# Kernel tuning notes

Hardware: AMD Instinct MI355X
Metric: run time of the kernel (lower is better)

Reference implementation:

```python
import jax, jax.numpy as jnp
import numpy as np

D_MODEL = 1024
N_HEADS = 16
HEAD_DIM = D_MODEL // N_HEADS
B, S = 2, 2048


def setup_inputs() -> dict:
    key = jax.random.key(0)
    ks = jax.random.split(key, 6)
    w_scale = 1.0 / np.sqrt(D_MODEL)
    return {
        "query": jax.random.normal(ks[0], (B, S, D_MODEL), dtype=jnp.float32),
        "Wq": jax.random.normal(ks[1], (D_MODEL, D_MODEL), dtype=jnp.float32) * w_scale,
        "Wk": jax.random.normal(ks[2], (D_MODEL, D_MODEL), dtype=jnp.float32) * w_scale,
        "Wv": jax.random.normal(ks[3], (D_MODEL, D_MODEL), dtype=jnp.float32) * w_scale,
        "Wo": jax.random.normal(ks[4], (D_MODEL, D_MODEL), dtype=jnp.float32) * w_scale,
        "bo": jnp.zeros((D_MODEL,), dtype=jnp.float32),
    }


def reference(query, Wq, Wk, Wv, Wo, bo):
    # Self-attention: key = value = query (forward() defaults).
    b, t, _ = query.shape
    # Q/K/V projections (nn.Linear applies x @ W.T; weights here are stored as
    # [out, in] like torch, so project with W.T). Split into heads: [B,H,T,Dh].
    def proj(x, W):
        return (x @ W.T).reshape(b, t, N_HEADS, HEAD_DIM).transpose(0, 2, 1, 3)

    q = proj(query, Wq)
    k = proj(query, Wk)
    v = proj(query, Wv)

    scale = 1.0 / np.sqrt(HEAD_DIM)
    scores = jnp.einsum("bhqd,bhkd->bhqk", q, k) * scale  # [B,H,T,T]
    # Causal mask (is_causal=True, not cross-attention).
    causal = jnp.tril(jnp.ones((t, t), dtype=bool))
    scores = jnp.where(causal, scores, jnp.finfo(scores.dtype).min)
    weights = jax.nn.softmax(scores, axis=-1)
    out = jnp.einsum("bhqk,bhkd->bhqd", weights, v)  # [B,H,T,Dh]
    out = out.transpose(0, 2, 1, 3).reshape(b, t, D_MODEL)
    # Output projection with bias (dropout is identity in eval mode).
    return out @ Wo.T + bo
```

## Files before the change

### kernel.cpp

```cpp
#include <hip/hip_runtime.h>
#include <hip/hip_bf16.h>
#include <math.h>

typedef __attribute__((ext_vector_type(8))) short short8;
typedef __attribute__((ext_vector_type(4))) float floatx4;
typedef __attribute__((ext_vector_type(2))) _Float16 half2v;
typedef __attribute__((ext_vector_type(4))) _Float16 half4v;

#define MFMA_BF16_32(a, b, c) __builtin_amdgcn_mfma_f32_16x16x32_bf16(a, b, c, 0, 0, 0)
#define MFMA_F16_16(a, b, c) __builtin_amdgcn_mfma_f32_16x16x16f16(a, b, c, 0, 0, 0)

static constexpr int NH = 16;
static constexpr int Bb = 2;
static constexpr int Ss = 2048;
static constexpr int DM = 1024;

__device__ inline unsigned short f2bf(float f) {
    unsigned int u = __float_as_uint(f);
    u += 0x7fffu + ((u >> 16) & 1u);
    return (unsigned short)(u >> 16);
}

__device__ __forceinline__ half2v pkrtz(float a, float b) {
    return __builtin_bit_cast(half2v, __builtin_amdgcn_cvt_pkrtz(a, b));
}

__device__ __forceinline__ void gload_lds16(const unsigned short* g, unsigned short* l) {
    __builtin_amdgcn_global_load_lds(
        (const __attribute__((address_space(1))) unsigned int*)g,
        (__attribute__((address_space(3))) unsigned int*)l, 16, 0, 0);
}

__global__ void convert_all(const float* __restrict__ X, const float* __restrict__ w0,
                            const float* __restrict__ w1, const float* __restrict__ w2,
                            const float* __restrict__ w3, unsigned short* __restrict__ dstX,
                            unsigned short* __restrict__ dstW) {
    const int bid = blockIdx.x;
    const float* src;
    unsigned short* dst;
    int i;
    if (bid < 4096) {
        src = X; dst = dstX; i = bid * 256 + threadIdx.x;
    } else {
        const int w = (bid - 4096) >> 10;
        src = (w == 0) ? w0 : (w == 1) ? w1 : (w == 2) ? w2 : w3;
        dst = dstW + (size_t)w * 1048576;
        i = ((bid - 4096) & 1023) * 256 + threadIdx.x;
    }
    float4 v = ((const float4*)src)[i];
    ushort4 o;
    o.x = f2bf(v.x); o.y = f2bf(v.y); o.z = f2bf(v.z); o.w = f2bf(v.w);
    ((ushort4*)dst)[i] = o;
}

__global__ __launch_bounds__(256) void gemm_qkv(const unsigned short* __restrict__ A,
                                                const unsigned short* __restrict__ Bm,
                                                unsigned short* __restrict__ Qp,
                                                unsigned short* __restrict__ Kp,
                                                unsigned short* __restrict__ Vt) {
    __shared__ __align__(16) unsigned short As[2][4096];
    __shared__ __align__(16) unsigned short Bs[2][4096];
    const int K = 1024;
    const int tid = threadIdx.x;
    const int wave = tid >> 6, lane = tid & 63;
    const int quad = lane >> 4, l16 = lane & 15;
    const int wr = wave >> 1, wc = wave & 1;

    const int l = blockIdx.x;
    const int xcd = l & 7, slot = l >> 3;
    const int bx = (xcd & 3) * 8 + (slot & 7);
    const int by = (xcd >> 2) * 12 + (slot >> 3);
    const int bm = bx * 128;
    const int bn = by * 128;

    const int s0 = wave * 64 + lane;
    const int srow = s0 >> 2;
    const int scg = (s0 & 3) ^ ((srow >> 1) & 3);
    const unsigned short* gA0 = A + (size_t)(bm + srow) * K + scg * 8;
    const unsigned short* gB0 = Bm + (size_t)(bn + srow) * K + scg * 8;

    auto stage = [&](int k0, int buf) {
        gload_lds16(gA0 + k0, &As[buf][wave * 512]);
        gload_lds16(gA0 + (size_t)64 * K + k0, &As[buf][2048 + wave * 512]);
        gload_lds16(gB0 + k0, &Bs[buf][wave * 512]);
        gload_lds16(gB0 + (size_t)64 * K + k0, &Bs[buf][2048 + wave * 512]);
    };

    floatx4 acc[4][4];
#pragma unroll
    for (int i = 0; i < 4; i++)
#pragma unroll
        for (int j = 0; j < 4; j++) acc[i][j] = (floatx4)0.0f;

    stage(0, 0);
    int buf = 0;
    for (int k0 = 0; k0 < K; k0 += 32) {
        __syncthreads();
        if (k0 + 32 < K) stage(k0 + 32, buf ^ 1);
        short8 af[4];
#pragma unroll
        for (int im = 0; im < 4; im++) {
            const int frow = wr * 64 + im * 16 + l16;
            af[im] = *(const short8*)&As[buf][frow * 32 + ((quad ^ ((frow >> 1) & 3)) * 8)];
        }
#pragma unroll
        for (int jn = 0; jn < 4; jn++) {
            const int frow = wc * 64 + jn * 16 + l16;
            short8 bf = *(const short8*)&Bs[buf][frow * 32 + ((quad ^ ((frow >> 1) & 3)) * 8)];
#pragma unroll
            for (int im = 0; im < 4; im++) acc[im][jn] = MFMA_BF16_32(af[im], bf, acc[im][jn]);
        }
        buf ^= 1;
    }
    __syncthreads();

    unsigned short* LB = &As[0][0];

    if (by < 16) {
        unsigned short* dst = (by < 8) ? Qp : Kp;
        const int nb = (by & 7) * 128;
        const float scale = (by < 8) ? 0.125f : 1.0f;
#pragma unroll
        for (int hf = 0; hf < 2; ++hf) {
            if (wc == hf) {
#pragma unroll
                for (int im = 0; im < 4; im++)
#pragma unroll
                    for (int jn = 0; jn < 4; jn++) {
                        const int row = wr * 64 + im * 16 + quad * 4;
                        const int col = jn * 16 + l16;
#pragma unroll
                        for (int r = 0; r < 4; r++)
                            LB[(row + r) * 64 + col] = f2bf(acc[im][jn][r] * scale);
                    }
            }
            __syncthreads();
#pragma unroll
            for (int i = 0; i < 4; ++i) {
                const int flat = i * 256 + tid;
                const int row = flat >> 3, ch = flat & 7;
                short8 v = *(const short8*)&LB[row * 64 + ch * 8];
                *(short8*)&dst[(size_t)(bm + row) * 1024 + nb + hf * 64 + ch * 8] = v;
            }
            __syncthreads();
        }
    } else {
        _Float16* LF = (_Float16*)LB;
        const int dbase = (by - 16) * 128;
        const int bI = bm >> 11, sbase = bm & 2047;
#pragma unroll
        for (int hf = 0; hf < 2; ++hf) {
            if (wc == hf) {
#pragma unroll
                for (int im = 0; im < 4; im++)
#pragma unroll
                    for (int jn = 0; jn < 4; jn++) {
                        const int d64 = jn * 16 + l16;
                        const int sl = wr * 64 + im * 16 + quad * 4;
                        *(half2v*)&LF[d64 * 128 + sl] = pkrtz(acc[im][jn][0], acc[im][jn][1]);
                        *(half2v*)&LF[d64 * 128 + sl + 2] = pkrtz(acc[im][jn][2], acc[im][jn][3]);
                    }
            }
            __syncthreads();
#pragma unroll
            for (int i = 0; i < 4; ++i) {
                const int flat = i * 256 + tid;
                const int dr = flat >> 4, ch = flat & 15;
                short8 v = *(const short8*)&LF[dr * 128 + ch * 8];
                const int d = dbase + hf * 64 + dr;
                const int head = d >> 6, d64g = d & 63;
                *(short8*)&Vt[(((size_t)(bI * 16 + head)) * 64 + d64g) * 2048 + sbase + ch * 8] = v;
            }
            __syncthreads();
        }
    }
}

__global__ __launch_bounds__(256) void gemm_out(const unsigned short* __restrict__ A,
                                                const unsigned short* __restrict__ Bm,
                                                float* __restrict__ C,
                                                const float* __restrict__ bias) {
    __shared__ __align__(16) unsigned short As[2][8192];
    __shared__ __align__(16) unsigned short Bs[2][4096];
    const int K = 1024;
    const int tid = threadIdx.x;
    const int wave = tid >> 6, lane = tid & 63;
    const int quad = lane >> 4, l16 = lane & 15;

    const int l = blockIdx.x;
    const int xcd = l & 7, slot = l >> 3;
    const int bx = (xcd & 3) * 8 + (slot & 7);
    const int by = (xcd >> 2) * 8 + (slot >> 3);
    const int bm = bx * 128, bn = by * 64;

    const int s0 = wave * 64 + lane;
    const int srow = s0 >> 2;
    const int scg = (s0 & 3) ^ ((srow >> 1) & 3);
    const unsigned short* gA0 = A + (size_t)(bm + srow) * K + scg * 8;
    const unsigned short* gB0 = Bm + (size_t)(bn + srow) * K + scg * 8;

    auto stage = [&](int k0, int buf) {
#pragma unroll
        for (int kh = 0; kh < 2; ++kh) {
            gload_lds16(gA0 + k0 + kh * 32, &As[buf][kh * 4096 + wave * 512]);
            gload_lds16(gA0 + (size_t)64 * K + k0 + kh * 32,
                        &As[buf][kh * 4096 + 2048 + wave * 512]);
            gload_lds16(gB0 + k0 + kh * 32, &Bs[buf][kh * 2048 + wave * 512]);
        }
    };

    floatx4 acc[2][4];
#pragma unroll
    for (int i = 0; i < 2; i++)
#pragma unroll
        for (int j = 0; j < 4; j++) acc[i][j] = (floatx4)0.0f;

    stage(0, 0);
    int buf = 0;
    for (int k0 = 0; k0 < K; k0 += 64) {
        __syncthreads();
        if (k0 + 64 < K) stage(k0 + 64, buf ^ 1);
#pragma unroll
        for (int kh = 0; kh < 2; ++kh) {
            const int abase = kh * 4096, bbase = kh * 2048;
            short8 af[2];
#pragma unroll
            for (int im = 0; im < 2; im++) {
                const int frow = wave * 32 + im * 16 + l16;
                af[im] = *(const short8*)&As[buf][abase + frow * 32 +
                                                  ((quad ^ ((frow >> 1) & 3)) * 8)];
            }
#pragma unroll
            for (int jn = 0; jn < 4; jn++) {
                const int frow = jn * 16 + l16;
                short8 bf = *(const short8*)&Bs[buf][bbase + frow * 32 +
                                                     ((quad ^ ((frow >> 1) & 3)) * 8)];
#pragma unroll
                for (int im = 0; im < 2; im++) acc[im][jn] = MFMA_BF16_32(af[im], bf, acc[im][jn]);
            }
        }
        buf ^= 1;
    }

#pragma unroll
    for (int im = 0; im < 2; im++) {
#pragma unroll
        for (int jn = 0; jn < 4; jn++) {
            const int row0 = bm + wave * 32 + im * 16 + quad * 4;
            const int colg = bn + jn * 16 + l16;
            const float bv = bias[colg];
#pragma unroll
            for (int r = 0; r < 4; r++)
                C[(size_t)(row0 + r) * 1024 + colg] = acc[im][jn][r] + bv;
        }
    }
}

__global__ __launch_bounds__(256) void flash_attn(const unsigned short* __restrict__ Qp,
                                                  const unsigned short* __restrict__ Kp,
                                                  const _Float16* __restrict__ Vt,
                                                  unsigned short* __restrict__ Out) {
    __shared__ __align__(16) unsigned short Ks[2][4096];
    __shared__ __align__(16) _Float16 Vs[2][4096];
    const int bx = blockIdx.x, h = blockIdx.y, b = blockIdx.z;
    int qt = (bx + h) & 15;
    if (b) qt = 15 - qt;
    const int tid = threadIdx.x, w = tid >> 6, lane = tid & 63;
    const int quad = lane >> 4, l16 = lane & 15;

    const int t8 = tid >> 3;
    const int cg = (tid & 7) ^ (t8 & 7);
    const unsigned short* gK0 = Kp + ((size_t)(b * 2048 + t8) << 10) + h * 64 + cg * 8;
    const unsigned short* gK1 = gK0 + ((size_t)32 << 10);
    const _Float16* gV0 = Vt + ((size_t)((b * 16 + h) * 64 + t8) << 11) + cg * 8;
    const _Float16* gV1 = gV0 + ((size_t)32 << 11);
    unsigned short* ldsK = &Ks[0][0] + w * 512;
    _Float16* ldsV = &Vs[0][0] + w * 512;

    auto stage = [&](int kt, int buf) {
        const size_t ko = (size_t)kt << 16;
        const size_t vo = (size_t)kt << 6;
        gload_lds16(gK0 + ko, ldsK + buf * 4096);
        gload_lds16(gK1 + ko, ldsK + buf * 4096 + 2048);
        gload_lds16((const unsigned short*)(gV0 + vo), (unsigned short*)(ldsV + buf * 4096));
        gload_lds16((const unsigned short*)(gV1 + vo), (unsigned short*)(ldsV + buf * 4096 + 2048));
    };

    stage(0, 0);

    short8 qfA[2], qfB[2];
    {
        const unsigned short* qa =
            Qp + ((size_t)(b * 2048 + qt * 128 + w * 16 + l16) << 10) + h * 64 + quad * 8;
        qfA[0] = *(const short8*)qa;
        qfA[1] = *(const short8*)(qa + 32);
        const unsigned short* qb = qa + ((size_t)64 << 10);
        qfB[0] = *(const short8*)qb;
        qfB[1] = *(const short8*)(qb + 32);
    }

    floatx4 accA[4], accB[4];
#pragma unroll
    for (int dt = 0; dt < 4; dt++) { accA[dt] = (floatx4)0.0f; accB[dt] = (floatx4)0.0f; }
    float lA = 0.0f, lB = 0.0f;
    const int qloc = w * 16 + l16;
    const int sw = l16 & 7;
    const int ktEnd = 2 * qt + 1;

    for (int kt = 0; kt <= ktEnd; ++kt) {
        __syncthreads();
        const int buf = kt & 1;
        if (kt < ktEnd) stage(kt + 1, buf ^ 1);
        const bool aAct = (kt <= 2 * qt);
        const bool aDiag = (kt == 2 * qt);
        const bool bDiag = (kt == ktEnd);
        const unsigned short* KB = &Ks[buf][0];
        const _Float16* VB = &Vs[buf][0];

#pragma unroll
        for (int sc = 0; sc < 4; ++sc) {
            const int rowk = sc * 16 + l16;
            short8 kf0 = *(const short8*)&KB[rowk * 64 + ((quad ^ sw) * 8)];
            short8 kf1 = *(const short8*)&KB[rowk * 64 + (((4 + quad) ^ sw) * 8)];

            half4v pA, pB;
            if (aAct) {
                floatx4 sA = MFMA_BF16_32(kf0, qfA[0], (floatx4)(-2.0f));
                sA = MFMA_BF16_32(kf1, qfA[1], sA);
                float ps[4];
#pragma unroll
                for (int r = 0; r < 4; ++r) {
                    float e = __expf(sA[r]);
                    if (aDiag && (sc * 16 + quad * 4 + r > qloc)) e = 0.0f;
                    ps[r] = e;
                }
                lA += (ps[0] + ps[1]) + (ps[2] + ps[3]);
                pA = __builtin_shufflevector(pkrtz(ps[0], ps[1]), pkrtz(ps[2], ps[3]), 0, 1, 2, 3);
            }
            {
                floatx4 sB = MFMA_BF16_32(kf0, qfB[0], (floatx4)(-2.0f));
                sB = MFMA_BF16_32(kf1, qfB[1], sB);
                float ps[4];
#pragma unroll
                for (int r = 0; r < 4; ++r) {
                    float e = __expf(sB[r]);
                    if (bDiag && (sc * 16 + quad * 4 + r > qloc)) e = 0.0f;
                    ps[r] = e;
                }
                lB += (ps[0] + ps[1]) + (ps[2] + ps[3]);
                pB = __builtin_shufflevector(pkrtz(ps[0], ps[1]), pkrtz(ps[2], ps[3]), 0, 1, 2, 3);
            }

#pragma unroll
            for (int dt = 0; dt < 4; ++dt) {
                const int rowv = dt * 16 + l16;
                const int cgv = ((sc * 2 + (quad >> 1)) ^ sw);
                half4v vf = *(const half4v*)&VB[rowv * 64 + cgv * 8 + (quad & 1) * 4];
                if (aAct) accA[dt] = MFMA_F16_16(vf, pA, accA[dt]);
                accB[dt] = MFMA_F16_16(vf, pB, accB[dt]);
            }
        }
    }

    lA += __shfl_xor(lA, 16); lA += __shfl_xor(lA, 32);
    lB += __shfl_xor(lB, 16); lB += __shfl_xor(lB, 32);
    const float iA = 1.0f / lA;
    const float iB = 1.0f / lB;

    const size_t rowA = (size_t)(b * 2048 + qt * 128 + w * 16 + l16);
    const size_t rowB = rowA + 64;
#pragma unroll
    for (int dt = 0; dt < 4; ++dt) {
        const int col = h * 64 + dt * 16 + quad * 4;
        ushort4 oa, ob;
        oa.x = f2bf(accA[dt][0] * iA); oa.y = f2bf(accA[dt][1] * iA);
        oa.z = f2bf(accA[dt][2] * iA); oa.w = f2bf(accA[dt][3] * iA);
        ob.x = f2bf(accB[dt][0] * iB); ob.y = f2bf(accB[dt][1] * iB);
        ob.z = f2bf(accB[dt][2] * iB); ob.w = f2bf(accB[dt][3] * iB);
        *(ushort4*)&Out[rowA * 1024 + col] = oa;
        *(ushort4*)&Out[rowB * 1024 + col] = ob;
    }
}

extern "C" void kernel_launch(void* const* d_in, const int* in_sizes, int n_in,
                              void* d_out, int out_size, void* d_ws, size_t ws_size,
                              hipStream_t stream) {
    const float* X  = (const float*)d_in[0];
    const float* Wq = (const float*)d_in[1];
    const float* Wk = (const float*)d_in[2];
    const float* Wv = (const float*)d_in[3];
    const float* Wo = (const float*)d_in[4];
    const float* bo = (const float*)d_in[5];

    unsigned short* ws = (unsigned short*)d_ws;
    unsigned short* Xb   = ws;
    unsigned short* W4   = ws + (size_t)4194304;
    unsigned short* Wob  = W4 + (size_t)3145728;
    unsigned short* Qp   = ws + (size_t)8388608;
    unsigned short* Kp   = ws + (size_t)12582912;
    unsigned short* Vt   = ws + (size_t)16777216;
    unsigned short* At   = ws + (size_t)20971520;

    convert_all<<<8192, 256, 0, stream>>>(X, Wq, Wk, Wv, Wo, Xb, W4);

    gemm_qkv<<<768, 256, 0, stream>>>(Xb, W4, Qp, Kp, Vt);

    flash_attn<<<dim3(16, NH, Bb), 256, 0, stream>>>(Qp, Kp, (const _Float16*)Vt, At);

    gemm_out<<<512, 256, 0, stream>>>(At, Wob, (float*)d_out, bo);
}
```

Before: 200.8 us.

## Triple-buffer LDS staging with vmcnt barriers and XCD-aware attention block mapping

Converts the double-buffered global-to-LDS pipelines in both GEMMs and flash attention to triple buffering. The full __syncthreads is replaced by an s_waitcnt vmcnt(N)+s_barrier so loads two stages ahead can stay in flight. This aims to hide memory latency behind the MFMA work. The attention launch also becomes a 1D grid remapped so each XCD handles whole (batch, head) pairs with balanced causal work. The cost is more LDS per block, which may reduce occupancy, and the code now relies on exact vmcnt counts.

```diff
diff --git a/kernel.cpp b/kernel.cpp
--- a/kernel.cpp
+++ b/kernel.cpp
@@ -9,6 +9,10 @@
 
 #define MFMA_BF16_32(a, b, c) __builtin_amdgcn_mfma_f32_16x16x32_bf16(a, b, c, 0, 0, 0)
 #define MFMA_F16_16(a, b, c) __builtin_amdgcn_mfma_f32_16x16x16f16(a, b, c, 0, 0, 0)
+
+#define PIPE_BAR4() asm volatile("s_waitcnt vmcnt(4)\n\ts_barrier" ::: "memory")
+#define PIPE_BAR6() asm volatile("s_waitcnt vmcnt(6)\n\ts_barrier" ::: "memory")
+#define PIPE_BAR0() asm volatile("s_waitcnt vmcnt(0)\n\ts_barrier" ::: "memory")
 
 static constexpr int NH = 16;
 static constexpr int Bb = 2;
@@ -58,8 +62,8 @@
                                                 unsigned short* __restrict__ Qp,
                                                 unsigned short* __restrict__ Kp,
                                                 unsigned short* __restrict__ Vt) {
-    __shared__ __align__(16) unsigned short As[2][4096];
-    __shared__ __align__(16) unsigned short Bs[2][4096];
+    __shared__ __align__(16) unsigned short As[3][4096];
+    __shared__ __align__(16) unsigned short Bs[3][4096];
     const int K = 1024;
     const int tid = threadIdx.x;
     const int wave = tid >> 6, lane = tid & 63;
@@ -93,10 +97,13 @@
         for (int j = 0; j < 4; j++) acc[i][j] = (floatx4)0.0f;
 
     stage(0, 0);
+    stage(32, 1);
     int buf = 0;
     for (int k0 = 0; k0 < K; k0 += 32) {
-        __syncthreads();
-        if (k0 + 32 < K) stage(k0 + 32, buf ^ 1);
+        if (k0 + 32 < K) { PIPE_BAR4(); } else { PIPE_BAR0(); }
+        const int nbuf = (buf == 2) ? 0 : buf + 1;
+        const int pbuf = (nbuf == 2) ? 0 : nbuf + 1;
+        if (k0 + 64 < K) stage(k0 + 64, pbuf);
         short8 af[4];
 #pragma unroll
         for (int im = 0; im < 4; im++) {
@@ -110,7 +117,7 @@
 #pragma unroll
             for (int im = 0; im < 4; im++) acc[im][jn] = MFMA_BF16_32(af[im], bf, acc[im][jn]);
         }
-        buf ^= 1;
+        buf = nbuf;
     }
     __syncthreads();
 
@@ -180,8 +187,8 @@
                                                 const unsigned short* __restrict__ Bm,
                                                 float* __restrict__ C,
                                                 const float* __restrict__ bias) {
-    __shared__ __align__(16) unsigned short As[2][8192];
-    __shared__ __align__(16) unsigned short Bs[2][4096];
+    __shared__ __align__(16) unsigned short As[3][8192];
+    __shared__ __align__(16) unsigned short Bs[3][4096];
     const int K = 1024;
     const int tid = threadIdx.x;
     const int wave = tid >> 6, lane = tid & 63;
@@ -216,10 +223,13 @@
         for (int j = 0; j < 4; j++) acc[i][j] = (floatx4)0.0f;
 
     stage(0, 0);
+    stage(64, 1);
     int buf = 0;
     for (int k0 = 0; k0 < K; k0 += 64) {
-        __syncthreads();
-        if (k0 + 64 < K) stage(k0 + 64, buf ^ 1);
+        if (k0 + 64 < K) { PIPE_BAR6(); } else { PIPE_BAR0(); }
+        const int nbuf = (buf == 2) ? 0 : buf + 1;
+        const int pbuf = (nbuf == 2) ? 0 : nbuf + 1;
+        if (k0 + 128 < K) stage(k0 + 128, pbuf);
 #pragma unroll
         for (int kh = 0; kh < 2; ++kh) {
             const int abase = kh * 4096, bbase = kh * 2048;
@@ -239,7 +249,7 @@
                 for (int im = 0; im < 2; im++) acc[im][jn] = MFMA_BF16_32(af[im], bf, acc[im][jn]);
             }
         }
-        buf ^= 1;
+        buf = nbuf;
     }
 
 #pragma unroll
@@ -260,33 +270,18 @@
                                                   const unsigned short* __restrict__ Kp,
                                                   const _Float16* __restrict__ Vt,
                                                   unsigned short* __restrict__ Out) {
-    __shared__ __align__(16) unsigned short Ks[2][4096];
-    __shared__ __align__(16) _Float16 Vs[2][4096];
-    const int bx = blockIdx.x, h = blockIdx.y, b = blockIdx.z;
-    int qt = (bx + h) & 15;
-    if (b) qt = 15 - qt;
+    __shared__ __align__(16) unsigned short Ks[3][4096];
+    __shared__ __align__(16) _Float16 Vs[3][4096];
+    const int lin = blockIdx.x;
+    const int xcd = lin & 7, slot = lin >> 3;
+    const int pr = slot >> 4;
+    const int pair = xcd * 4 + pr;
+    const int h = pair & 15, b = pair >> 4;
+    const int qt0 = slot & 15;
+    const int qt = (pr & 1) ? 15 - qt0 : qt0;
+
     const int tid = threadIdx.x, w = tid >> 6, lane = tid & 63;
     const int quad = lane >> 4, l16 = lane & 15;
-
-    const int t8 = tid >> 3;
-    const int cg = (tid & 7) ^ (t8 & 7);
-    const unsigned short* gK0 = Kp + ((size_t)(b * 2048 + t8) << 10) + h * 64 + cg * 8;
-    const unsigned short* gK1 = gK0 + ((size_t)32 << 10);
-    const _Float16* gV0 = Vt + ((size_t)((b * 16 + h) * 64 + t8) << 11) + cg * 8;
-    const _Float16* gV1 = gV0 + ((size_t)32 << 11);
-    unsigned short* ldsK = &Ks[0][0] + w * 512;
-    _Float16* ldsV = &Vs[0][0] + w * 512;
-
-    auto stage = [&](int kt, int buf) {
-        const size_t ko = (size_t)kt << 16;
-        const size_t vo = (size_t)kt << 6;
-        gload_lds16(gK0 + ko, ldsK + buf * 4096);
-        gload_lds16(gK1 + ko, ldsK + buf * 4096 + 2048);
-        gload_lds16((const unsigned short*)(gV0 + vo), (unsigned short*)(ldsV + buf * 4096));
-        gload_lds16((const unsigned short*)(gV1 + vo), (unsigned short*)(ldsV + buf * 4096 + 2048));
-    };
-
-    stage(0, 0);
 
     short8 qfA[2], qfB[2];
     {
@@ -299,18 +294,41 @@
         qfB[1] = *(const short8*)(qb + 32);
     }
 
+    const int t8 = tid >> 3;
+    const int cg = (tid & 7) ^ (t8 & 7);
+    const unsigned short* gK0 = Kp + ((size_t)(b * 2048 + t8) << 10) + h * 64 + cg * 8;
+    const unsigned short* gK1 = gK0 + ((size_t)32 << 10);
+    const _Float16* gV0 = Vt + ((size_t)((b * 16 + h) * 64 + t8) << 11) + cg * 8;
+    const _Float16* gV1 = gV0 + ((size_t)32 << 11);
+    unsigned short* ldsK = &Ks[0][0] + w * 512;
+    _Float16* ldsV = &Vs[0][0] + w * 512;
+
+    auto stage = [&](int kt, int buf) {
+        const size_t ko = (size_t)kt << 16;
+        const size_t vo = (size_t)kt << 6;
+        gload_lds16(gK0 + ko, ldsK + buf * 4096);
+        gload_lds16(gK1 + ko, ldsK + buf * 4096 + 2048);
+        gload_lds16((const unsigned short*)(gV0 + vo), (unsigned short*)(ldsV + buf * 4096));
+        gload_lds16((const unsigned short*)(gV1 + vo), (unsigned short*)(ldsV + buf * 4096 + 2048));
+    };
+
+    const int ktEnd = 2 * qt + 1;
+    stage(0, 0);
+    stage(1, 1);
+
     floatx4 accA[4], accB[4];
 #pragma unroll
     for (int dt = 0; dt < 4; dt++) { accA[dt] = (floatx4)0.0f; accB[dt] = (floatx4)0.0f; }
     float lA = 0.0f, lB = 0.0f;
     const int qloc = w * 16 + l16;
     const int sw = l16 & 7;
-    const int ktEnd = 2 * qt + 1;
-
+
+    int buf = 0;
     for (int kt = 0; kt <= ktEnd; ++kt) {
-        __syncthreads();
-        const int buf = kt & 1;
-        if (kt < ktEnd) stage(kt + 1, buf ^ 1);
+        if (kt < ktEnd) { PIPE_BAR4(); } else { PIPE_BAR0(); }
+        const int nbuf = (buf == 2) ? 0 : buf + 1;
+        const int pbuf = (nbuf == 2) ? 0 : nbuf + 1;
+        if (kt + 2 <= ktEnd) stage(kt + 2, pbuf);
         const bool aAct = (kt <= 2 * qt);
         const bool aDiag = (kt == 2 * qt);
         const bool bDiag = (kt == ktEnd);
@@ -360,6 +378,7 @@
                 accB[dt] = MFMA_F16_16(vf, pB, accB[dt]);
             }
         }
+        buf = nbuf;
     }
 
     lA += __shfl_xor(lA, 16); lA += __shfl_xor(lA, 32);
@@ -405,7 +424,7 @@
 
     gemm_qkv<<<768, 256, 0, stream>>>(Xb, W4, Qp, Kp, Vt);
 
-    flash_attn<<<dim3(16, NH, Bb), 256, 0, stream>>>(Qp, Kp, (const _Float16*)Vt, At);
+    flash_attn<<<512, 256, 0, stream>>>(Qp, Kp, (const _Float16*)Vt, At);
 
     gemm_out<<<512, 256, 0, stream>>>(At, Wob, (float*)d_out, bo);
 }
```

Result: slower. 204.8 us (+2.0%).
